# Kernel optimization log

Measured on AMD Instinct MI355X. Metric: run time of the kernel, lower is better.

The kernel has to match this reference:

```python
import math
import jax, jax.numpy as jnp
import numpy as np

B = 8          # number of graphs in the batch
NMAX = 256     # max nodes per graph (padding size)
K = 128        # num_kernels
H = 32         # num_heads
NTYPE = 101    # max_node_type + 1


def setup_inputs() -> dict:
    key = jax.random.key(0)
    ks = jax.random.split(key, 10)
    sizes = np.asarray(NMAX - np.arange(B) * 16, dtype=np.int32)  # 256,240,...,144 -> ragged
    N = int(sizes.sum())  # 1600
    coord = jax.random.normal(ks[0], (N, 3), dtype=jnp.float32) * 3.0
    node_type = jax.random.randint(ks[1], (N,), 0, NTYPE, dtype=jnp.int32)
    gaussian_means = jax.random.uniform(ks[2], (1, K), minval=0.0, maxval=3.0, dtype=jnp.float32)
    gaussian_stds = jax.random.uniform(ks[3], (1, K), minval=0.0, maxval=3.0, dtype=jnp.float32)
    # nn.Embedding(max_node_type+1, 2) tables; original init is const(0)/const(1),
    # we perturb so the computation is non-degenerate.
    mul_w = jax.random.normal(ks[4], (NTYPE, 2), dtype=jnp.float32) * 0.1
    bias_w = 1.0 + jax.random.normal(ks[5], (NTYPE, 2), dtype=jnp.float32) * 0.1
    W1 = jax.random.normal(ks[6], (K, K), dtype=jnp.float32) / math.sqrt(K)
    b1 = jnp.zeros((K,), dtype=jnp.float32)
    W2 = jax.random.normal(ks[7], (K, H), dtype=jnp.float32) / math.sqrt(K)
    b2 = jnp.zeros((H,), dtype=jnp.float32)
    return {
        "coord": coord,
        "gaussian_means": gaussian_means,
        "gaussian_stds": gaussian_stds,
        "mul_w": mul_w,
        "bias_w": bias_w,
        "W1": W1,
        "b1": b1,
        "W2": W2,
        "b2": b2,
        "node_type": node_type,
        "batch_num_nodes": jnp.asarray(sizes),
    }


def reference(coord, gaussian_means, gaussian_stds, mul_w, bias_w, W1, b1, W2, b2,
              node_type, batch_num_nodes):
    N = coord.shape[0]
    offsets = jnp.concatenate([jnp.zeros((1,), dtype=batch_num_nodes.dtype),
                               jnp.cumsum(batch_num_nodes)[:-1]])
    ar = jnp.arange(NMAX)
    idx = offsets[:, None] + ar[None, :]                     # [B, n] flat node index per graph slot
    valid = ar[None, :] < batch_num_nodes[:, None]           # [B, n] node mask
    idx_c = jnp.clip(idx, 0, N - 1)
    pc = coord[idx_c]                                        # [B, n, 3] padded coords
    pt = node_type[idx_c]                                    # [B, n]

    # pairwise Euclidean distance (torch.cdist p=2), sqrt-safe at 0
    diff = pc[:, :, None, :] - pc[:, None, :, :]             # [B, n, n, 3]
    sq = jnp.sum(diff * diff, axis=-1)                       # [B, n, n]
    nz = sq > 0
    dist = jnp.where(nz, jnp.sqrt(jnp.where(nz, sq, 1.0)), 0.0)

    # outer-sum of per-node (src, dst) scaling embeddings
    mul_e = mul_w[pt]                                        # [B, n, 2]
    bias_e = bias_w[pt]
    mul = mul_e[:, :, None, 0] + mul_e[:, None, :, 1]        # [B, n, n]
    bias = bias_e[:, :, None, 0] + bias_e[:, None, :, 1]
    scaled = mul * dist + bias                               # [B, n, n]

    means = gaussian_means.reshape(-1)                       # [K]
    stds = jnp.abs(gaussian_stds.reshape(-1)) + 0.01         # [K]
    z = (scaled[..., None] - means) / stds                   # [B, n, n, K]
    gk = jnp.exp(-0.5 * z * z) / (-math.sqrt(2.0 * math.pi) * stds)

    h = jax.nn.gelu(gk @ W1 + b1, approximate=False)         # exact gelu like torch F.gelu
    out = h @ W2 + b2                                        # [B, n, n, H]

    pair = valid[:, :, None] & valid[:, None, :]             # padded positions -> -inf
    return jnp.where(pair[..., None], out, -jnp.inf)
```

## Files before the change

kernel.cpp:

```cpp
#include <hip/hip_runtime.h>
#include <math.h>

#define NMAXC 256
#define KC 128
#define HC 32
#define BC 8
#define TP 128
#define NEG_SENTINEL (-1.0e30f)
#define LOG2E 1.4426950408889634f

typedef __bf16 bf16x8 __attribute__((ext_vector_type(8)));
typedef float  f32x16 __attribute__((ext_vector_type(16)));
union FragU { uint4 u; bf16x8 v; };

#define EXP2F(x) __builtin_amdgcn_exp2f(x)

__device__ __forceinline__ unsigned pack2(float lo, float hi) {
    return __builtin_amdgcn_perm(__float_as_uint(hi), __float_as_uint(lo), 0x07060302u);
}

__global__ __launch_bounds__(256) void se3d_prep(const float* __restrict__ W1,
                                                 const float* __restrict__ W2,
                                                 const float* __restrict__ gm,
                                                 const float* __restrict__ gs,
                                                 unsigned* __restrict__ wsu) {
    int t = blockIdx.x * 256 + threadIdx.x;
    if (t < 2048) {
        int f = t >> 6, l = t & 63;
        int mt = f >> 3, ks = f & 7;
        int c  = mt * 32 + (l & 31);
        int k0 = ks * 16 + 8 * (l >> 5);
        unsigned u[4];
#pragma unroll
        for (int p = 0; p < 4; ++p)
            u[p] = pack2(-W1[(k0 + 2 * p) * KC + c], -W1[(k0 + 2 * p + 1) * KC + c]);
        ((uint4*)wsu)[t] = make_uint4(u[0], u[1], u[2], u[3]);
    } else if (t < 2560) {
        int x = t - 2048;
        int ft = x >> 6, l = x & 63;
        int hi = l >> 5, ln = l & 31;
        unsigned u[4];
#pragma unroll
        for (int d = 0; d < 4; ++d) {
            int c0 = 32 * (ft >> 1) + 16 * (ft & 1) + 8 * (d >> 1) + 4 * hi + 2 * (d & 1);
            u[d] = pack2(W2[c0 * HC + ln], W2[(c0 + 1) * HC + ln]);
        }
        ((uint4*)wsu)[2048 + x] = make_uint4(u[0], u[1], u[2], u[3]);
    } else if (t < 2688) {
        int k = t - 2560;
        float inv = 1.0f / (fabsf(gs[k]) + 0.01f);
        float m   = gm[k];
        float A2  = -0.5f * inv * inv * LOG2E;
        float* wf = (float*)wsu + 10240;
        wf[k]       = A2;
        wf[128 + k] = -2.0f * A2 * m;
        wf[256 + k] = A2 * m * m + log2f(0.3989422804014327f * inv);
    }
}

__global__ __launch_bounds__(256, 4) void se3d_main(
    const float* __restrict__ coord, const float* __restrict__ mulw,
    const float* __restrict__ biasw, const float* __restrict__ b1,
    const float* __restrict__ b2, const int* __restrict__ ntype,
    const int* __restrict__ bnn, const void* __restrict__ ws,
    float* __restrict__ out)
{
    __shared__ __attribute__((aligned(16))) float cst[544];

    const int b = blockIdx.y;
    const int n = bnn[b];
    const int q0 = blockIdx.x * TP;
    const int tid = threadIdx.x;

    if (q0 >= n * n) {
        int v = q0 + (tid >> 1) - n * n;
        int wdt = 256 - n;
        int na = n * wdt;
        int i, j;
        if (v < na) { i = v / wdt; j = n + (v - i * wdt); }
        else        { int vp = v - na; i = n + (vp >> 8); j = vp & 255; }
        float4 s4 = make_float4(NEG_SENTINEL, NEG_SENTINEL, NEG_SENTINEL, NEG_SENTINEL);
        float4* o = (float4*)(out + ((size_t)((b * NMAXC + i) * NMAXC + j)) * HC)
                  + (tid & 1) * 4;
#pragma unroll
        for (int t = 0; t < 4; ++t) o[t] = s4;
        return;
    }

    if (tid < 136) {
        uint4 v;
        if (tid < 96)       v = ((const uint4*)((const char*)ws + 40960))[tid];
        else if (tid < 128) v = ((const uint4*)b1)[tid - 96];
        else                v = ((const uint4*)b2)[tid - 128];
        ((uint4*)cst)[tid] = v;
    }
    int off = 0;
    for (int t = 0; t < b; ++t) off += bnn[t];
    __syncthreads();

    const int l = tid & 63, w = tid >> 6;
    const int hi = l >> 5, ln = l & 31;

    int q = q0 + w * 32 + ln;
    int i = q / n;
    int j = q - i * n;
    int gi = off + i, gj = off + j;
    float dx = coord[gi * 3 + 0] - coord[gj * 3 + 0];
    float dy = coord[gi * 3 + 1] - coord[gj * 3 + 1];
    float dz = coord[gi * 3 + 2] - coord[gj * 3 + 2];
    float sq = dx * dx + dy * dy + dz * dz;
    float dist = sq > 0.f ? sqrtf(sq) : 0.f;
    int ti = ntype[gi], tj = ntype[gj];
    float s = (mulw[ti * 2 + 0] + mulw[tj * 2 + 1]) * dist
            + (biasw[ti * 2 + 0] + biasw[tj * 2 + 1]);
    size_t obase = ((size_t)((b * NMAXC + i) * NMAXC + j)) * HC;

    const float4*  c4  = (const float4*)cst;
    const bf16x8*  w1t = (const bf16x8*)ws;
    const bf16x8*  w2t = (const bf16x8*)((const char*)ws + 32768);

    f32x16 acc[4];
#pragma unroll
    for (int nt = 0; nt < 4; ++nt)
#pragma unroll
        for (int qd = 0; qd < 4; ++qd) {
            float4 bv = c4[96 + 8 * nt + 2 * qd + hi];
            acc[nt][4 * qd + 0] = bv.x; acc[nt][4 * qd + 1] = bv.y;
            acc[nt][4 * qd + 2] = bv.z; acc[nt][4 * qd + 3] = bv.w;
        }

#pragma unroll
    for (int ks = 0; ks < 8; ++ks) {
        int b4 = 4 * ks + 2 * hi;
        float4 a0 = c4[b4],      a1 = c4[b4 + 1];
        float4 p0 = c4[32 + b4], p1 = c4[32 + b4 + 1];
        float4 c0 = c4[64 + b4], c1 = c4[64 + b4 + 1];
        float g[8];
        g[0] = EXP2F(fmaf(fmaf(a0.x, s, p0.x), s, c0.x));
        g[1] = EXP2F(fmaf(fmaf(a0.y, s, p0.y), s, c0.y));
        g[2] = EXP2F(fmaf(fmaf(a0.z, s, p0.z), s, c0.z));
        g[3] = EXP2F(fmaf(fmaf(a0.w, s, p0.w), s, c0.w));
        g[4] = EXP2F(fmaf(fmaf(a1.x, s, p1.x), s, c1.x));
        g[5] = EXP2F(fmaf(fmaf(a1.y, s, p1.y), s, c1.y));
        g[6] = EXP2F(fmaf(fmaf(a1.z, s, p1.z), s, c1.z));
        g[7] = EXP2F(fmaf(fmaf(a1.w, s, p1.w), s, c1.w));
        FragU gf;
        gf.u.x = pack2(g[0], g[1]);
        gf.u.y = pack2(g[2], g[3]);
        gf.u.z = pack2(g[4], g[5]);
        gf.u.w = pack2(g[6], g[7]);
#pragma unroll
        for (int mt = 0; mt < 4; ++mt) {
            bf16x8 af = w1t[(mt * 8 + ks) * 64 + l];
            acc[mt] = __builtin_amdgcn_mfma_f32_32x32x16_bf16(af, gf.v, acc[mt], 0, 0, 0);
        }
    }

    const float KSG = -1.702f * LOG2E;
    unsigned hpk[32];
#pragma unroll
    for (int nt = 0; nt < 4; ++nt)
#pragma unroll
        for (int g8 = 0; g8 < 8; ++g8) {
            float x0 = acc[nt][2 * g8], x1 = acc[nt][2 * g8 + 1];
            float gl0 = x0 * __builtin_amdgcn_rcpf(1.0f + EXP2F(x0 * KSG));
            float gl1 = x1 * __builtin_amdgcn_rcpf(1.0f + EXP2F(x1 * KSG));
            hpk[nt * 8 + g8] = pack2(gl0, gl1);
        }

    f32x16 c2;
#pragma unroll
    for (int qd = 0; qd < 4; ++qd) {
        float4 bv = c4[128 + 2 * qd + hi];
        c2[4 * qd + 0] = bv.x; c2[4 * qd + 1] = bv.y;
        c2[4 * qd + 2] = bv.z; c2[4 * qd + 3] = bv.w;
    }
#pragma unroll
    for (int t = 0; t < 8; ++t) {
        FragU hf;
        int hb = 8 * (t >> 1) + 4 * (t & 1);
        hf.u = make_uint4(hpk[hb], hpk[hb + 1], hpk[hb + 2], hpk[hb + 3]);
        bf16x8 a2 = w2t[t * 64 + l];
        c2 = __builtin_amdgcn_mfma_f32_32x32x16_bf16(a2, hf.v, c2, 0, 0, 0);
    }

#pragma unroll
    for (int qd = 0; qd < 4; ++qd) {
        float4 v = make_float4(c2[4 * qd], c2[4 * qd + 1], c2[4 * qd + 2], c2[4 * qd + 3]);
        *(float4*)(out + obase + 8 * qd + 4 * hi) = v;
    }
}

extern "C" void kernel_launch(void* const* d_in, const int* in_sizes, int n_in,
                              void* d_out, int out_size, void* d_ws, size_t ws_size,
                              hipStream_t stream) {
    const float* coord = (const float*)d_in[0];
    const float* gm    = (const float*)d_in[1];
    const float* gs    = (const float*)d_in[2];
    const float* mulw  = (const float*)d_in[3];
    const float* biasw = (const float*)d_in[4];
    const float* W1    = (const float*)d_in[5];
    const float* b1    = (const float*)d_in[6];
    const float* W2    = (const float*)d_in[7];
    const float* b2    = (const float*)d_in[8];
    const int* ntype   = (const int*)d_in[9];
    const int* bnn     = (const int*)d_in[10];
    float* out = (float*)d_out;

    hipLaunchKernelGGL(se3d_prep, dim3(11), dim3(256), 0, stream,
                       W1, W2, gm, gs, (unsigned*)d_ws);
    hipLaunchKernelGGL(se3d_main, dim3(NMAXC * NMAXC / TP, BC), dim3(256),
                       0, stream,
                       coord, mulw, biasw, b1, b2, ntype, bnn, d_ws, out);
}
```

Measured before the change: 125.3 us.

## Restructure MLP loops to stream hidden tiles through second GEMM

The loop order changes: all eight Gaussian basis fragments are computed up front, then for each of the four hidden column tiles the first GEMM is accumulated, GELU is applied and the result is fed straight into the second GEMM. Only one 16-float accumulator is live instead of four, which cuts register pressure and may allow more waves per SIMD or avoid spills. The cost is that the MFMA chain for each tile is now a serial dependency of eight, and GELU work sits between MFMA bursts, so there is less independent MFMA work to hide latency.

```diff
diff --git a/kernel.cpp b/kernel.cpp
--- a/kernel.cpp
+++ b/kernel.cpp
@@ -119,54 +119,26 @@
     const bf16x8*  w1t = (const bf16x8*)ws;
     const bf16x8*  w2t = (const bf16x8*)((const char*)ws + 32768);
 
-    f32x16 acc[4];
-#pragma unroll
-    for (int nt = 0; nt < 4; ++nt)
-#pragma unroll
-        for (int qd = 0; qd < 4; ++qd) {
-            float4 bv = c4[96 + 8 * nt + 2 * qd + hi];
-            acc[nt][4 * qd + 0] = bv.x; acc[nt][4 * qd + 1] = bv.y;
-            acc[nt][4 * qd + 2] = bv.z; acc[nt][4 * qd + 3] = bv.w;
-        }
-
+    FragU gf[8];
 #pragma unroll
     for (int ks = 0; ks < 8; ++ks) {
         int b4 = 4 * ks + 2 * hi;
         float4 a0 = c4[b4],      a1 = c4[b4 + 1];
         float4 p0 = c4[32 + b4], p1 = c4[32 + b4 + 1];
         float4 c0 = c4[64 + b4], c1 = c4[64 + b4 + 1];
-        float g[8];
-        g[0] = EXP2F(fmaf(fmaf(a0.x, s, p0.x), s, c0.x));
-        g[1] = EXP2F(fmaf(fmaf(a0.y, s, p0.y), s, c0.y));
-        g[2] = EXP2F(fmaf(fmaf(a0.z, s, p0.z), s, c0.z));
-        g[3] = EXP2F(fmaf(fmaf(a0.w, s, p0.w), s, c0.w));
-        g[4] = EXP2F(fmaf(fmaf(a1.x, s, p1.x), s, c1.x));
-        g[5] = EXP2F(fmaf(fmaf(a1.y, s, p1.y), s, c1.y));
-        g[6] = EXP2F(fmaf(fmaf(a1.z, s, p1.z), s, c1.z));
-        g[7] = EXP2F(fmaf(fmaf(a1.w, s, p1.w), s, c1.w));
-        FragU gf;
-        gf.u.x = pack2(g[0], g[1]);
-        gf.u.y = pack2(g[2], g[3]);
-        gf.u.z = pack2(g[4], g[5]);
-        gf.u.w = pack2(g[6], g[7]);
-#pragma unroll
-        for (int mt = 0; mt < 4; ++mt) {
-            bf16x8 af = w1t[(mt * 8 + ks) * 64 + l];
-            acc[mt] = __builtin_amdgcn_mfma_f32_32x32x16_bf16(af, gf.v, acc[mt], 0, 0, 0);
-        }
-    }
-
-    const float KSG = -1.702f * LOG2E;
-    unsigned hpk[32];
-#pragma unroll
-    for (int nt = 0; nt < 4; ++nt)
-#pragma unroll
-        for (int g8 = 0; g8 < 8; ++g8) {
-            float x0 = acc[nt][2 * g8], x1 = acc[nt][2 * g8 + 1];
-            float gl0 = x0 * __builtin_amdgcn_rcpf(1.0f + EXP2F(x0 * KSG));
-            float gl1 = x1 * __builtin_amdgcn_rcpf(1.0f + EXP2F(x1 * KSG));
-            hpk[nt * 8 + g8] = pack2(gl0, gl1);
-        }
+        float g0 = EXP2F(fmaf(fmaf(a0.x, s, p0.x), s, c0.x));
+        float g1 = EXP2F(fmaf(fmaf(a0.y, s, p0.y), s, c0.y));
+        float g2 = EXP2F(fmaf(fmaf(a0.z, s, p0.z), s, c0.z));
+        float g3 = EXP2F(fmaf(fmaf(a0.w, s, p0.w), s, c0.w));
+        float g4 = EXP2F(fmaf(fmaf(a1.x, s, p1.x), s, c1.x));
+        float g5 = EXP2F(fmaf(fmaf(a1.y, s, p1.y), s, c1.y));
+        float g6 = EXP2F(fmaf(fmaf(a1.z, s, p1.z), s, c1.z));
+        float g7 = EXP2F(fmaf(fmaf(a1.w, s, p1.w), s, c1.w));
+        gf[ks].u.x = pack2(g0, g1);
+        gf[ks].u.y = pack2(g2, g3);
+        gf[ks].u.z = pack2(g4, g5);
+        gf[ks].u.w = pack2(g6, g7);
+    }
 
     f32x16 c2;
 #pragma unroll
@@ -175,13 +147,36 @@
         c2[4 * qd + 0] = bv.x; c2[4 * qd + 1] = bv.y;
         c2[4 * qd + 2] = bv.z; c2[4 * qd + 3] = bv.w;
     }
-#pragma unroll
-    for (int t = 0; t < 8; ++t) {
-        FragU hf;
-        int hb = 8 * (t >> 1) + 4 * (t & 1);
-        hf.u = make_uint4(hpk[hb], hpk[hb + 1], hpk[hb + 2], hpk[hb + 3]);
-        bf16x8 a2 = w2t[t * 64 + l];
-        c2 = __builtin_amdgcn_mfma_f32_32x32x16_bf16(a2, hf.v, c2, 0, 0, 0);
+
+    const float KSG = -1.702f * LOG2E;
+
+#pragma unroll
+    for (int nt = 0; nt < 4; ++nt) {
+        f32x16 acc;
+#pragma unroll
+        for (int qd = 0; qd < 4; ++qd) {
+            float4 bv = c4[96 + 8 * nt + 2 * qd + hi];
+            acc[4 * qd + 0] = bv.x; acc[4 * qd + 1] = bv.y;
+            acc[4 * qd + 2] = bv.z; acc[4 * qd + 3] = bv.w;
+        }
+#pragma unroll
+        for (int ks = 0; ks < 8; ++ks) {
+            bf16x8 af = w1t[(nt * 8 + ks) * 64 + l];
+            acc = __builtin_amdgcn_mfma_f32_32x32x16_bf16(af, gf[ks].v, acc, 0, 0, 0);
+        }
+        unsigned hpk8[8];
+#pragma unroll
+        for (int g8 = 0; g8 < 8; ++g8) {
+            float x0 = acc[2 * g8], x1 = acc[2 * g8 + 1];
+            float gl0 = x0 * __builtin_amdgcn_rcpf(1.0f + EXP2F(x0 * KSG));
+            float gl1 = x1 * __builtin_amdgcn_rcpf(1.0f + EXP2F(x1 * KSG));
+            hpk8[g8] = pack2(gl0, gl1);
+        }
+        FragU hf0, hf1;
+        hf0.u = make_uint4(hpk8[0], hpk8[1], hpk8[2], hpk8[3]);
+        hf1.u = make_uint4(hpk8[4], hpk8[5], hpk8[6], hpk8[7]);
+        c2 = __builtin_amdgcn_mfma_f32_32x32x16_bf16(w2t[(2 * nt) * 64 + l], hf0.v, c2, 0, 0, 0);
+        c2 = __builtin_amdgcn_mfma_f32_32x32x16_bf16(w2t[(2 * nt + 1) * 64 + l], hf1.v, c2, 0, 0, 0);
     }
 
 #pragma unroll
```

Result: no change. 126.0 us (+0.5%).
